# Kernel tuning notes

Hardware: AMD Instinct MI355X
Metric: run time of the kernel (lower is better)

The kernel has to match this reference:

```python
import jax, jax.numpy as jnp
import numpy as np
from jax import lax

A_PLUS = 0.01
A_MINUS = 0.01
TAU_PLUS = 20.0
TAU_MINUS = 20.0
W_MAX = 1.0
W_MIN = 0.0

B, T, PRE_N, POST_N = 16, 128, 2048, 2048


def setup_inputs() -> dict:
    key = jax.random.key(0)
    k1, k2, k3 = jax.random.split(key, 3)
    weights = jax.random.uniform(k1, (POST_N, PRE_N), dtype=jnp.float32)
    pre_spikes = jax.random.uniform(k2, (B, T, PRE_N), dtype=jnp.float32)
    post_spikes = jax.random.uniform(k3, (B, T, POST_N), dtype=jnp.float32)
    return {"weights": weights, "pre_spikes": pre_spikes,
            "post_spikes": post_spikes, "dt": 1}


def compute_trace(spikes, tau, dt):
    # Faithful to torch loop: trace[:,0,:] = 0; trace[t] = decay*trace[t-1] + spikes[t] for t>=1
    decay = jnp.exp(jnp.float32(-dt / tau))
    s_tb = jnp.swapaxes(spikes, 0, 1)  # [T, B, N]
    init = jnp.zeros_like(s_tb[0])

    def step(carry, s_t):
        tr = decay * carry + s_t
        return tr, tr

    _, tr = lax.scan(step, init, s_tb[1:])          # [T-1, B, N]
    tr = jnp.concatenate([init[None], tr], axis=0)  # [T, B, N]
    return jnp.swapaxes(tr, 0, 1)                   # [B, T, N]


def reference(weights, pre_spikes, post_spikes, dt):
    batch = pre_spikes.shape[0]
    pre_trace = compute_trace(pre_spikes, TAU_PLUS, dt)
    post_trace = compute_trace(post_spikes, TAU_MINUS, dt)

    # sum over t of mean over batch of outer products -> single contraction over (b, t)
    # ltp[q,p] = A_plus * sum_t mean_b post_spikes[b,t,q] * pre_trace[b,t,p]
    ltp = A_PLUS * jnp.einsum('btq,btp->qp', post_spikes, pre_trace) / batch
    # ltd[q,p] = -A_minus * sum_t mean_b post_trace[b,t,q] * pre_spikes[b,t,p]
    ltd = -A_MINUS * jnp.einsum('btq,btp->qp', post_trace, pre_spikes) / batch

    # softbound weight dependence (constant in t, distributes over the sum)
    w_factor = (W_MAX - weights) * (weights - W_MIN) / ((W_MAX - W_MIN) / 2) ** 2
    delta_w = w_factor * (ltp + ltd)
    return delta_w
```

## Files before the change

kernel.cpp:

```cpp
#include <hip/hip_runtime.h>
#include <hip/hip_bf16.h>


typedef __attribute__((ext_vector_type(8))) short bf16x8;
typedef __attribute__((ext_vector_type(4))) float f32x4;

#define GN 2048
#define KTOT 2048
#define A_SCALE (0.01f / 16.0f)
#define FST 68
#define ZST 66
#define RST 36

#define GLOAD_LDS16(gp, lp) \
    __builtin_amdgcn_global_load_lds((const __attribute__((address_space(1))) void*)(gp), \
                                     (__attribute__((address_space(3))) void*)(lp), 16, 0, 0)

__device__ __forceinline__ unsigned bf16bits(float x) {
    __hip_bfloat16 h = __float2bfloat16(x);
    return (unsigned)*(unsigned short*)&h;
}

__global__ __launch_bounds__(256, 4) void trace_kernel(
    const float* __restrict__ pre,
    const float* __restrict__ post,
    const int* __restrict__ dtp,
    __hip_bfloat16* __restrict__ AT,
    __hip_bfloat16* __restrict__ BT)
{
    __shared__ float fbuf[128 * FST];
    __hip_bfloat16* zbuf = (__hip_bfloat16*)fbuf;

    const int tid = threadIdx.x;
    const int w   = tid >> 6;
    const int l   = tid & 63;
    const int nq  = tid & 15;
    const int tl  = tid >> 4;
    const int n0  = blockIdx.x * 64;
    const int b   = blockIdx.y;
    const int a   = blockIdx.z;

    int di = dtp[0];
    float dtf = (di > 0 && di < 1000000) ? (float)di : *(const float*)dtp;
    const float decay = __expf(-dtf / 20.0f);

    if (a == 0) {
        #pragma unroll
        for (int pass = 0; pass < 8; ++pass) {
            const int t = pass * 16 + tl;
            float4 v = *(const float4*)&post[((size_t)b * 128 + t) * GN + n0 + 4 * nq];
            uint2 pk;
            pk.x = bf16bits(v.x) | (bf16bits(v.y) << 16);
            pk.y = bf16bits(v.z) | (bf16bits(v.w) << 16);
            *(uint2*)&zbuf[t * ZST + 4 * nq] = pk;
        }
        __syncthreads();
    } else {
        #pragma unroll
        for (int pass = 0; pass < 8; ++pass) {
            const int t = pass * 16 + tl;
            float4 v = *(const float4*)&pre[((size_t)b * 128 + t) * GN + n0 + 4 * nq];
            *(float4*)&fbuf[t * FST + 4 * nq] = v;
        }
        __syncthreads();

        const int t0 = 32 * w;
        float carry = 0.0f;
        #pragma unroll 8
        for (int t = 1; t < t0; ++t)
            carry = decay * carry + fbuf[t * FST + l];
        float z[32];
        #pragma unroll
        for (int j = 0; j < 32; ++j) {
            const int t = t0 + j;
            if (t >= 1) carry = decay * carry + fbuf[t * FST + l];
            z[j] = carry;
        }
        float bc = 0.0f;
        #pragma unroll 8
        for (int t = 127; t >= t0 + 32; --t)
            bc = decay * bc + fbuf[t * FST + l];
        #pragma unroll
        for (int j = 31; j >= 0; --j) {
            const int t = t0 + j;
            bc = decay * bc + fbuf[t * FST + l];
            if (t >= 1) z[j] -= bc;
        }
        __syncthreads();
        #pragma unroll
        for (int j = 0; j < 32; ++j)
            zbuf[(t0 + j) * ZST + l] = __float2bfloat16(z[j]);
        __syncthreads();
    }

    __hip_bfloat16* dst = (a == 0) ? AT : BT;
    #pragma unroll
    for (int j = 0; j < 4; ++j) {
        const int c  = tid + 256 * j;
        const int n  = c >> 4;
        const int tc = c & 15;
        unsigned int vv[8];
        #pragma unroll
        for (int i = 0; i < 8; ++i)
            vv[i] = *(const unsigned short*)&zbuf[(8 * tc + i) * ZST + n];
        uint4 pk;
        pk.x = vv[0] | (vv[1] << 16);
        pk.y = vv[2] | (vv[3] << 16);
        pk.z = vv[4] | (vv[5] << 16);
        pk.w = vv[6] | (vv[7] << 16);
        *(uint4*)(dst + (size_t)(n0 + n) * KTOT + b * 128 + tc * 8) = pk;
    }
}

__global__ __launch_bounds__(512) void stdp_gemm(
    const __hip_bfloat16* __restrict__ AT,
    const __hip_bfloat16* __restrict__ BT,
    const float* __restrict__ W,
    float* __restrict__ out)
{
    __shared__ alignas(16) char smem[49152];

    const int tid  = threadIdx.x;
    const int lane = tid & 63;
    const int wv8  = tid >> 6;
    const int grp  = wv8 >> 2;
    const int wv   = wv8 & 3;
    const int wm   = (wv >> 1) * 64;
    const int wn   = (wv & 1) * 32;
    const int RM   = blockIdx.y * 128;
    const int CN   = blockIdx.x * 64;
    const int l15  = lane & 15;
    const int quad = lane >> 4;

    __hip_bfloat16* Ag = (__hip_bfloat16*)(smem + grp * 24576);
    __hip_bfloat16* Bg = (__hip_bfloat16*)(smem + grp * 24576 + 16384);

    f32x4 acc[4][2] = {};

    const int K0 = grp * 1024;
    for (int k0 = K0; k0 < K0 + 1024; k0 += 64) {
        __syncthreads();
        #pragma unroll
        for (int it = 0; it < 4; ++it) {
            const int cbase = it * 256 + wv * 64;
            const int c     = cbase + lane;
            const int row   = c >> 3;
            const int kc    = (c & 7) ^ (row & 7);
            GLOAD_LDS16(AT + (size_t)(RM + row) * KTOT + k0 + kc * 8, Ag + (size_t)cbase * 8);
        }
        #pragma unroll
        for (int it = 0; it < 2; ++it) {
            const int cbase = it * 256 + wv * 64;
            const int c     = cbase + lane;
            const int row   = c >> 3;
            const int kc    = (c & 7) ^ (row & 7);
            GLOAD_LDS16(BT + (size_t)(CN + row) * KTOT + k0 + kc * 8, Bg + (size_t)cbase * 8);
        }
        __syncthreads();

        #pragma unroll
        for (int kk = 0; kk < 64; kk += 32) {
            const int jg = (kk >> 3) + quad;
            bf16x8 af[4], bfr[2];
            #pragma unroll
            for (int i = 0; i < 4; ++i) {
                const int mr = wm + i * 16 + l15;
                af[i] = *(const bf16x8*)(Ag + mr * 64 + ((jg ^ (mr & 7)) * 8));
            }
            #pragma unroll
            for (int j = 0; j < 2; ++j) {
                const int nr = wn + j * 16 + l15;
                bfr[j] = *(const bf16x8*)(Bg + nr * 64 + ((jg ^ (nr & 7)) * 8));
            }
            #pragma unroll
            for (int i = 0; i < 4; ++i)
                #pragma unroll
                for (int j = 0; j < 2; ++j)
                    acc[i][j] = __builtin_amdgcn_mfma_f32_16x16x32_bf16(
                        af[i], bfr[j], acc[i][j], 0, 0, 0);
        }
    }

    float* red = (float*)smem;
    const int rbase = wv * 64 * RST;
    __syncthreads();
    if (grp == 1) {
        #pragma unroll
        for (int i = 0; i < 4; ++i)
            #pragma unroll
            for (int r = 0; r < 4; ++r)
                #pragma unroll
                for (int j = 0; j < 2; ++j)
                    red[rbase + (i * 16 + quad * 4 + r) * RST + j * 16 + l15] = acc[i][j][r];
    }
    __syncthreads();
    if (grp == 0) {
        #pragma unroll
        for (int i = 0; i < 4; ++i) {
            #pragma unroll
            for (int r = 0; r < 4; ++r) {
                const int q = RM + wm + i * 16 + quad * 4 + r;
                #pragma unroll
                for (int j = 0; j < 2; ++j) {
                    const int p = CN + wn + j * 16 + l15;
                    float v = acc[i][j][r]
                            + red[rbase + (i * 16 + quad * 4 + r) * RST + j * 16 + l15];
                    const float w  = W[(size_t)q * GN + p];
                    const float wf = 4.0f * w * (1.0f - w);
                    out[(size_t)q * GN + p] = wf * A_SCALE * v;
                }
            }
        }
    }
}

extern "C" void kernel_launch(void* const* d_in, const int* in_sizes, int n_in,
                              void* d_out, int out_size, void* d_ws, size_t ws_size,
                              hipStream_t stream) {
    const float* W    = (const float*)d_in[0];
    const float* pre  = (const float*)d_in[1];
    const float* post = (const float*)d_in[2];
    const int*   dt   = (const int*)d_in[3];
    float* out = (float*)d_out;

    __hip_bfloat16* AT = (__hip_bfloat16*)d_ws;
    __hip_bfloat16* BT = AT + (size_t)GN * KTOT;

    trace_kernel<<<dim3(32, 16, 2), 256, 0, stream>>>(pre, post, dt, AT, BT);
    stdp_gemm<<<dim3(32, 16), 512, 0, stream>>>(AT, BT, W, out);
}
```

Measured before the change: 122.2 us.

## Double-buffer GEMM K-loop with 32-wide stages and swizzle tile order

```diff
diff --git a/kernel.cpp b/kernel.cpp
--- a/kernel.cpp
+++ b/kernel.cpp
@@ -112,7 +112,7 @@
     }
 }
 
-__global__ __launch_bounds__(512) void stdp_gemm(
+__global__ __launch_bounds__(512, 4) void stdp_gemm(
     const __hip_bfloat16* __restrict__ AT,
     const __hip_bfloat16* __restrict__ BT,
     const float* __restrict__ W,
@@ -127,63 +127,78 @@
     const int wv   = wv8 & 3;
     const int wm   = (wv >> 1) * 64;
     const int wn   = (wv & 1) * 32;
-    const int RM   = blockIdx.y * 128;
-    const int CN   = blockIdx.x * 64;
+
+    const int hw   = blockIdx.y * 32 + blockIdx.x;
+    const int tile = (hw & 7) * 64 + (hw >> 3);
+    const int RM   = (tile >> 5) * 128;
+    const int CN   = (tile & 31) * 64;
+
     const int l15  = lane & 15;
     const int quad = lane >> 4;
 
-    __hip_bfloat16* Ag = (__hip_bfloat16*)(smem + grp * 24576);
-    __hip_bfloat16* Bg = (__hip_bfloat16*)(smem + grp * 24576 + 16384);
+    char* base = smem + grp * 24576;
+
+    const int K0 = grp * 1024;
+
+    const int cA0   = wv * 64 + lane;
+    const int rowA0 = cA0 >> 2;
+    const int rowA1 = rowA0 + 64;
+    const int sl    = cA0 & 3;
+    const int swzA0 = (rowA0 ^ (rowA0 >> 2)) & 3;
+    const int swzA1 = (rowA1 ^ (rowA1 >> 2)) & 3;
+    const __hip_bfloat16* srcA0 = AT + (size_t)(RM + rowA0) * KTOT + (sl ^ swzA0) * 8;
+    const __hip_bfloat16* srcA1 = AT + (size_t)(RM + rowA1) * KTOT + (sl ^ swzA1) * 8;
+    const __hip_bfloat16* srcB  = BT + (size_t)(CN + rowA0) * KTOT + (sl ^ swzA0) * 8;
+
+    const int dA0 = wv * 1024;
+    const int dA1 = 4096 + wv * 1024;
+    const int dB  = wv * 1024;
+
+#define STAGE(buf, kofs) do {                                        \
+        char* Ab_ = base + (buf) * 12288;                            \
+        char* Bb_ = Ab_ + 8192;                                      \
+        GLOAD_LDS16(srcA0 + (kofs), Ab_ + dA0);                      \
+        GLOAD_LDS16(srcA1 + (kofs), Ab_ + dA1);                      \
+        GLOAD_LDS16(srcB  + (kofs), Bb_ + dB);                       \
+    } while (0)
 
     f32x4 acc[4][2] = {};
 
-    const int K0 = grp * 1024;
-    for (int k0 = K0; k0 < K0 + 1024; k0 += 64) {
-        __syncthreads();
-        #pragma unroll
-        for (int it = 0; it < 4; ++it) {
-            const int cbase = it * 256 + wv * 64;
-            const int c     = cbase + lane;
-            const int row   = c >> 3;
-            const int kc    = (c & 7) ^ (row & 7);
-            GLOAD_LDS16(AT + (size_t)(RM + row) * KTOT + k0 + kc * 8, Ag + (size_t)cbase * 8);
-        }
-        #pragma unroll
-        for (int it = 0; it < 2; ++it) {
-            const int cbase = it * 256 + wv * 64;
-            const int c     = cbase + lane;
-            const int row   = c >> 3;
-            const int kc    = (c & 7) ^ (row & 7);
-            GLOAD_LDS16(BT + (size_t)(CN + row) * KTOT + k0 + kc * 8, Bg + (size_t)cbase * 8);
-        }
-        __syncthreads();
-
-        #pragma unroll
-        for (int kk = 0; kk < 64; kk += 32) {
-            const int jg = (kk >> 3) + quad;
-            bf16x8 af[4], bfr[2];
+    STAGE(0, K0);
+    __syncthreads();
+
+    #pragma unroll 2
+    for (int h = 0; h < 32; ++h) {
+        const int cur = h & 1;
+        if (h < 31) STAGE(cur ^ 1, K0 + (h + 1) * 32);
+
+        const __hip_bfloat16* Ag = (const __hip_bfloat16*)(base + cur * 12288);
+        const __hip_bfloat16* Bg = Ag + 4096;
+
+        bf16x8 af[4], bfr[2];
+        #pragma unroll
+        for (int i = 0; i < 4; ++i) {
+            const int mr = wm + i * 16 + l15;
+            af[i] = *(const bf16x8*)(Ag + mr * 32 + ((quad ^ ((mr ^ (mr >> 2)) & 3)) * 8));
+        }
+        #pragma unroll
+        for (int j = 0; j < 2; ++j) {
+            const int nr = wn + j * 16 + l15;
+            bfr[j] = *(const bf16x8*)(Bg + nr * 32 + ((quad ^ ((nr ^ (nr >> 2)) & 3)) * 8));
+        }
+        #pragma unroll
+        for (int i = 0; i < 4; ++i)
             #pragma unroll
-            for (int i = 0; i < 4; ++i) {
-                const int mr = wm + i * 16 + l15;
-                af[i] = *(const bf16x8*)(Ag + mr * 64 + ((jg ^ (mr & 7)) * 8));
-            }
-            #pragma unroll
-            for (int j = 0; j < 2; ++j) {
-                const int nr = wn + j * 16 + l15;
-                bfr[j] = *(const bf16x8*)(Bg + nr * 64 + ((jg ^ (nr & 7)) * 8));
-            }
-            #pragma unroll
-            for (int i = 0; i < 4; ++i)
-                #pragma unroll
-                for (int j = 0; j < 2; ++j)
-                    acc[i][j] = __builtin_amdgcn_mfma_f32_16x16x32_bf16(
-                        af[i], bfr[j], acc[i][j], 0, 0, 0);
-        }
-    }
+            for (int j = 0; j < 2; ++j)
+                acc[i][j] = __builtin_amdgcn_mfma_f32_16x16x32_bf16(
+                    af[i], bfr[j], acc[i][j], 0, 0, 0);
+
+        __syncthreads();
+    }
+#undef STAGE
 
     float* red = (float*)smem;
     const int rbase = wv * 64 * RST;
-    __syncthreads();
     if (grp == 1) {
         #pragma unroll
         for (int i = 0; i < 4; ++i)
```

After: 133.7 us. 1.09x slower.

## Double-buffer A tiles in LDS, load B directly to registers, remap block order

Applied to the files above, without the earlier changes.

```diff
diff --git a/kernel.cpp b/kernel.cpp
--- a/kernel.cpp
+++ b/kernel.cpp
@@ -118,7 +118,7 @@
     const float* __restrict__ W,
     float* __restrict__ out)
 {
-    __shared__ alignas(16) char smem[49152];
+    __shared__ alignas(16) char smem[65536];
 
     const int tid  = threadIdx.x;
     const int lane = tid & 63;
@@ -127,63 +127,80 @@
     const int wv   = wv8 & 3;
     const int wm   = (wv >> 1) * 64;
     const int wn   = (wv & 1) * 32;
-    const int RM   = blockIdx.y * 128;
-    const int CN   = blockIdx.x * 64;
+
+    const int hw = blockIdx.y * 32 + blockIdx.x;
+    const int xc = hw & 7;
+    const int rr = hw >> 3;
+    const int CN = (xc * 4 + (rr & 3)) * 64;
+    const int RM = (rr >> 2) * 128;
+
     const int l15  = lane & 15;
     const int quad = lane >> 4;
 
-    __hip_bfloat16* Ag = (__hip_bfloat16*)(smem + grp * 24576);
-    __hip_bfloat16* Bg = (__hip_bfloat16*)(smem + grp * 24576 + 16384);
+    char* gbase = smem + grp * 32768;
+    const int K0 = grp * 1024;
+
+    const __hip_bfloat16* Bb = BT + (size_t)(CN + wn + l15) * KTOT + K0 + quad * 8;
+
+#define STAGE(buf, kofs) do {                                                  \
+        char* Ab_ = gbase + (buf) * 16384;                                     \
+        _Pragma("unroll")                                                      \
+        for (int it_ = 0; it_ < 4; ++it_) {                                    \
+            const int cbase_ = it_ * 256 + wv * 64;          \
+            const int c_     = cbase_ + lane;                                  \
+            const int row_   = c_ >> 3;                                        \
+            const int kc_    = (c_ & 7) ^ (row_ & 7);                          \
+            GLOAD_LDS16(AT + (size_t)(RM + row_) * KTOT + (kofs) + kc_ * 8,    \
+                        Ab_ + cbase_ * 16);                                    \
+        } } while (0)
 
     f32x4 acc[4][2] = {};
 
-    const int K0 = grp * 1024;
-    for (int k0 = K0; k0 < K0 + 1024; k0 += 64) {
-        __syncthreads();
-        #pragma unroll
-        for (int it = 0; it < 4; ++it) {
-            const int cbase = it * 256 + wv * 64;
-            const int c     = cbase + lane;
-            const int row   = c >> 3;
-            const int kc    = (c & 7) ^ (row & 7);
-            GLOAD_LDS16(AT + (size_t)(RM + row) * KTOT + k0 + kc * 8, Ag + (size_t)cbase * 8);
-        }
-        #pragma unroll
-        for (int it = 0; it < 2; ++it) {
-            const int cbase = it * 256 + wv * 64;
-            const int c     = cbase + lane;
-            const int row   = c >> 3;
-            const int kc    = (c & 7) ^ (row & 7);
-            GLOAD_LDS16(BT + (size_t)(CN + row) * KTOT + k0 + kc * 8, Bg + (size_t)cbase * 8);
-        }
-        __syncthreads();
-
-        #pragma unroll
-        for (int kk = 0; kk < 64; kk += 32) {
-            const int jg = (kk >> 3) + quad;
-            bf16x8 af[4], bfr[2];
-            #pragma unroll
-            for (int i = 0; i < 4; ++i) {
-                const int mr = wm + i * 16 + l15;
-                af[i] = *(const bf16x8*)(Ag + mr * 64 + ((jg ^ (mr & 7)) * 8));
-            }
-            #pragma unroll
-            for (int j = 0; j < 2; ++j) {
-                const int nr = wn + j * 16 + l15;
-                bfr[j] = *(const bf16x8*)(Bg + nr * 64 + ((jg ^ (nr & 7)) * 8));
-            }
-            #pragma unroll
-            for (int i = 0; i < 4; ++i)
-                #pragma unroll
-                for (int j = 0; j < 2; ++j)
-                    acc[i][j] = __builtin_amdgcn_mfma_f32_16x16x32_bf16(
-                        af[i], bfr[j], acc[i][j], 0, 0, 0);
-        }
-    }
+    STAGE(0, K0);
+    __syncthreads();
+
+    #pragma unroll 2
+    for (int h = 0; h < 16; ++h) {
+        const int cur  = h & 1;
+        const int kofs = K0 + h * 64;
+
+        bf16x8 b00 = *(const bf16x8*)(Bb + h * 64);
+        bf16x8 b01 = *(const bf16x8*)(Bb + 16 * KTOT + h * 64);
+        bf16x8 b10 = *(const bf16x8*)(Bb + 32 + h * 64);
+        bf16x8 b11 = *(const bf16x8*)(Bb + 16 * KTOT + 32 + h * 64);
+
+        if (h < 15) STAGE(cur ^ 1, kofs + 64);
+
+        const __hip_bfloat16* Ag = (const __hip_bfloat16*)(gbase + cur * 16384);
+
+        bf16x8 af[4];
+        #pragma unroll
+        for (int i = 0; i < 4; ++i) {
+            const int mr = wm + i * 16 + l15;
+            af[i] = *(const bf16x8*)(Ag + mr * 64 + ((quad ^ (mr & 7)) * 8));
+        }
+        #pragma unroll
+        for (int i = 0; i < 4; ++i) {
+            acc[i][0] = __builtin_amdgcn_mfma_f32_16x16x32_bf16(af[i], b00, acc[i][0], 0, 0, 0);
+            acc[i][1] = __builtin_amdgcn_mfma_f32_16x16x32_bf16(af[i], b01, acc[i][1], 0, 0, 0);
+        }
+        #pragma unroll
+        for (int i = 0; i < 4; ++i) {
+            const int mr = wm + i * 16 + l15;
+            af[i] = *(const bf16x8*)(Ag + mr * 64 + (((4 + quad) ^ (mr & 7)) * 8));
+        }
+        #pragma unroll
+        for (int i = 0; i < 4; ++i) {
+            acc[i][0] = __builtin_amdgcn_mfma_f32_16x16x32_bf16(af[i], b10, acc[i][0], 0, 0, 0);
+            acc[i][1] = __builtin_amdgcn_mfma_f32_16x16x32_bf16(af[i], b11, acc[i][1], 0, 0, 0);
+        }
+
+        __syncthreads();
+    }
+#undef STAGE
 
     float* red = (float*)smem;
     const int rbase = wv * 64 * RST;
-    __syncthreads();
     if (grp == 1) {
         #pragma unroll
         for (int i = 0; i < 4; ++i)
```

Result: slower. 138.8 us (+13.6%).

## Triple-buffer GEMM K-loop with 32x32 MFMA and drop split-K reduction

Applied to the files above, without the earlier changes.

```diff
diff --git a/kernel.cpp b/kernel.cpp
--- a/kernel.cpp
+++ b/kernel.cpp
@@ -3,14 +3,13 @@
 
 
 typedef __attribute__((ext_vector_type(8))) short bf16x8;
-typedef __attribute__((ext_vector_type(4))) float f32x4;
+typedef __attribute__((ext_vector_type(16))) float f32x16;
 
 #define GN 2048
 #define KTOT 2048
 #define A_SCALE (0.01f / 16.0f)
 #define FST 68
 #define ZST 66
-#define RST 36
 
 #define GLOAD_LDS16(gp, lp) \
     __builtin_amdgcn_global_load_lds((const __attribute__((address_space(1))) void*)(gp), \
@@ -112,105 +111,98 @@
     }
 }
 
-__global__ __launch_bounds__(512) void stdp_gemm(
+__global__ __launch_bounds__(512, 4) void stdp_gemm(
     const __hip_bfloat16* __restrict__ AT,
     const __hip_bfloat16* __restrict__ BT,
     const float* __restrict__ W,
     float* __restrict__ out)
 {
-    __shared__ alignas(16) char smem[49152];
+    __shared__ alignas(16) char smem[73728];
 
     const int tid  = threadIdx.x;
     const int lane = tid & 63;
     const int wv8  = tid >> 6;
-    const int grp  = wv8 >> 2;
-    const int wv   = wv8 & 3;
-    const int wm   = (wv >> 1) * 64;
-    const int wn   = (wv & 1) * 32;
+    const int wr   = wv8 >> 1;
+    const int wc   = wv8 & 1;
     const int RM   = blockIdx.y * 128;
     const int CN   = blockIdx.x * 64;
-    const int l15  = lane & 15;
-    const int quad = lane >> 4;
-
-    __hip_bfloat16* Ag = (__hip_bfloat16*)(smem + grp * 24576);
-    __hip_bfloat16* Bg = (__hip_bfloat16*)(smem + grp * 24576 + 16384);
-
-    f32x4 acc[4][2] = {};
-
-    const int K0 = grp * 1024;
-    for (int k0 = K0; k0 < K0 + 1024; k0 += 64) {
-        __syncthreads();
-        #pragma unroll
-        for (int it = 0; it < 4; ++it) {
-            const int cbase = it * 256 + wv * 64;
-            const int c     = cbase + lane;
-            const int row   = c >> 3;
-            const int kc    = (c & 7) ^ (row & 7);
-            GLOAD_LDS16(AT + (size_t)(RM + row) * KTOT + k0 + kc * 8, Ag + (size_t)cbase * 8);
-        }
-        #pragma unroll
-        for (int it = 0; it < 2; ++it) {
-            const int cbase = it * 256 + wv * 64;
-            const int c     = cbase + lane;
-            const int row   = c >> 3;
-            const int kc    = (c & 7) ^ (row & 7);
-            GLOAD_LDS16(BT + (size_t)(CN + row) * KTOT + k0 + kc * 8, Bg + (size_t)cbase * 8);
-        }
-        __syncthreads();
-
-        #pragma unroll
-        for (int kk = 0; kk < 64; kk += 32) {
-            const int jg = (kk >> 3) + quad;
-            bf16x8 af[4], bfr[2];
-            #pragma unroll
-            for (int i = 0; i < 4; ++i) {
-                const int mr = wm + i * 16 + l15;
-                af[i] = *(const bf16x8*)(Ag + mr * 64 + ((jg ^ (mr & 7)) * 8));
-            }
-            #pragma unroll
-            for (int j = 0; j < 2; ++j) {
-                const int nr = wn + j * 16 + l15;
-                bfr[j] = *(const bf16x8*)(Bg + nr * 64 + ((jg ^ (nr & 7)) * 8));
-            }
-            #pragma unroll
-            for (int i = 0; i < 4; ++i)
-                #pragma unroll
-                for (int j = 0; j < 2; ++j)
-                    acc[i][j] = __builtin_amdgcn_mfma_f32_16x16x32_bf16(
-                        af[i], bfr[j], acc[i][j], 0, 0, 0);
-        }
-    }
-
-    float* red = (float*)smem;
-    const int rbase = wv * 64 * RST;
-    __syncthreads();
-    if (grp == 1) {
-        #pragma unroll
-        for (int i = 0; i < 4; ++i)
-            #pragma unroll
-            for (int r = 0; r < 4; ++r)
-                #pragma unroll
-                for (int j = 0; j < 2; ++j)
-                    red[rbase + (i * 16 + quad * 4 + r) * RST + j * 16 + l15] = acc[i][j][r];
-    }
-    __syncthreads();
-    if (grp == 0) {
-        #pragma unroll
-        for (int i = 0; i < 4; ++i) {
-            #pragma unroll
-            for (int r = 0; r < 4; ++r) {
-                const int q = RM + wm + i * 16 + quad * 4 + r;
-                #pragma unroll
-                for (int j = 0; j < 2; ++j) {
-                    const int p = CN + wn + j * 16 + l15;
-                    float v = acc[i][j][r]
-                            + red[rbase + (i * 16 + quad * 4 + r) * RST + j * 16 + l15];
-                    const float w  = W[(size_t)q * GN + p];
-                    const float wf = 4.0f * w * (1.0f - w);
-                    out[(size_t)q * GN + p] = wf * A_SCALE * v;
-                }
-            }
-        }
+    const int l31  = lane & 31;
+    const int hi   = lane >> 5;
+
+    const int cS   = wv8 * 64 + lane;
+    const int rS   = cS >> 3;
+    const int sS   = cS & 7;
+    const int kc0  = sS ^ (rS & 7);
+    const int kc1  = sS ^ ((rS + 64) & 7);
+    const __hip_bfloat16* srcA0 = AT + (size_t)(RM + rS)      * KTOT + kc0 * 8;
+    const __hip_bfloat16* srcA1 = AT + (size_t)(RM + rS + 64) * KTOT + kc1 * 8;
+    const __hip_bfloat16* srcB  = BT + (size_t)(CN + rS)      * KTOT + kc0 * 8;
+    const int dS = wv8 * 1024;
+
+#define STAGE(BUF, kstep) do {                                   \
+        char* bb_ = (BUF);                                       \
+        const int ke_ = (kstep) * 64;                            \
+        GLOAD_LDS16(srcA0 + ke_, bb_ + dS);                      \
+        GLOAD_LDS16(srcA1 + ke_, bb_ + 8192 + dS);               \
+        GLOAD_LDS16(srcB  + ke_, bb_ + 16384 + dS);              \
+    } while (0)
+
+    const int ra = wr * 32 + l31;
+    const int rb = wc * 32 + l31;
+
+    f32x16 acc = {};
+
+#define COMPUTE(BUF) do {                                                       \
+        const __hip_bfloat16* Ab_ = (const __hip_bfloat16*)(BUF);               \
+        const __hip_bfloat16* Bb_ = (const __hip_bfloat16*)((BUF) + 16384);     \
+        bf16x8 av_[4], bv_[4];                                                  \
+        _Pragma("unroll")                                                       \
+        for (int ks_ = 0; ks_ < 4; ++ks_) {                                     \
+            const int ja_ = (ks_ * 2 + hi) ^ (ra & 7);                          \
+            const int jb_ = (ks_ * 2 + hi) ^ (rb & 7);                          \
+            av_[ks_] = *(const bf16x8*)(Ab_ + ra * 64 + ja_ * 8);               \
+            bv_[ks_] = *(const bf16x8*)(Bb_ + rb * 64 + jb_ * 8);               \
+        }                                                                       \
+        _Pragma("unroll")                                                       \
+        for (int ks_ = 0; ks_ < 4; ++ks_)                                       \
+            acc = __builtin_amdgcn_mfma_f32_32x32x16_bf16(av_[ks_], bv_[ks_],   \
+                                                          acc, 0, 0, 0);        \
+    } while (0)
+
+#define WAITBAR(N) do {                                          \
+        asm volatile("s_waitcnt vmcnt(" #N ")" ::: "memory");    \
+        __builtin_amdgcn_s_barrier();                            \
+        __builtin_amdgcn_sched_barrier(0);                       \
+    } while (0)
+
+    char* B0 = smem;
+    char* B1 = smem + 24576;
+    char* B2 = smem + 49152;
+
+    STAGE(B0, 0);
+    STAGE(B1, 1);
+    WAITBAR(3);
+
+    for (int hb = 0; hb < 30; hb += 3) {
+        STAGE(B2, hb + 2); COMPUTE(B0); WAITBAR(3);
+        STAGE(B0, hb + 3); COMPUTE(B1); WAITBAR(3);
+        STAGE(B1, hb + 4); COMPUTE(B2); WAITBAR(3);
+    }
+    COMPUTE(B0);
+    WAITBAR(0);
+    COMPUTE(B1);
+
+#undef STAGE
+#undef COMPUTE
+#undef WAITBAR
+
+    const int p = CN + wc * 32 + l31;
+    #pragma unroll
+    for (int r = 0; r < 16; ++r) {
+        const int q = RM + wr * 32 + (r & 3) + 8 * (r >> 2) + 4 * hi;
+        const float w  = W[(size_t)q * GN + p];
+        const float wf = 4.0f * w * (1.0f - w);
+        out[(size_t)q * GN + p] = wf * A_SCALE * acc[r];
     }
 }
 
```

Measured after the change: 119.3 us. 1.02x faster.
